# Performance work log

Measured on AMD Instinct MI355X. Metric: run time of the kernel, lower is better.

## Reference

```python
import jax, jax.numpy as jnp
import numpy as np

N_NODES = 50000
N_EDGES = 500000
D_MODEL = 128
D_INNER = 256
N_EXPERT = 64
TOP_K = 2
CAP_FACTOR = 2  # capacity factor for expert dispatch (fastmoe has no drop; factor 2 is ample for ~uniform gates)
BN_EPS = 1e-5


def setup_inputs() -> dict:
    key = jax.random.key(0)
    ks = jax.random.split(key, 12)
    d, h, E = D_MODEL, D_INNER, N_EXPERT
    return {
        "feats": jax.random.normal(ks[0], (N_NODES, d), jnp.float32),
        "edge_src": jax.random.randint(ks[1], (N_EDGES,), 0, N_NODES),
        "edge_dst": jax.random.randint(ks[2], (N_EDGES,), 0, N_NODES),
        "W_conv": jax.random.normal(ks[3], (d, d), jnp.float32) / np.sqrt(d),
        "b_conv": jnp.zeros((d,), jnp.float32),
        "gate_W": jax.random.normal(ks[4], (d, E), jnp.float32) / np.sqrt(d),
        "gate_b": jnp.zeros((E,), jnp.float32),
        "W1": jax.random.normal(ks[5], (E, d, h), jnp.float32) / np.sqrt(d),
        "b1": jnp.zeros((E, h), jnp.float32),
        "W2": jax.random.normal(ks[6], (E, h, d), jnp.float32) / np.sqrt(h),
        "b2": jnp.zeros((E, d), jnp.float32),
        "bn_gamma": jnp.ones((d,), jnp.float32),
        "bn_beta": jnp.zeros((d,), jnp.float32),
    }


def _gcn_conv(feats, edge_src, edge_dst, W_conv, b_conv):
    # symmetric-normalized sum aggregation over edge list
    n = feats.shape[0]
    ones = jnp.ones_like(edge_dst, dtype=feats.dtype)
    deg = jax.ops.segment_sum(ones, edge_dst, num_segments=n)
    deg = jnp.maximum(deg, 1.0)
    inv_sqrt = jax.lax.rsqrt(deg)
    norm = inv_sqrt[edge_src] * inv_sqrt[edge_dst]          # [Ed]
    msgs = feats[edge_src] * norm[:, None]                  # [Ed, d]
    agg = jax.ops.segment_sum(msgs, edge_dst, num_segments=n)
    return agg @ W_conv + b_conv


def _moe_ffn(x, gate_W, gate_b, W1, b1, W2, b2):
    # fastmoe NaiveGate: top-k of linear gate, softmax over the top-k scores
    T, d = x.shape
    E, h = W1.shape[0], W1.shape[2]
    scores = x @ gate_W + gate_b                            # [T, E]
    topv, topi = jax.lax.top_k(scores, TOP_K)               # [T, k]
    gw = jax.nn.softmax(topv, axis=-1)                      # [T, k]

    P = T * TOP_K
    eid = topi.reshape(P)                                   # expert id per (token, slot)
    x_rep = jnp.repeat(x, TOP_K, axis=0)                    # [P, d]

    onehot = jax.nn.one_hot(eid, E, dtype=jnp.int32)        # [P, E]
    pos = jnp.sum(jnp.cumsum(onehot, axis=0) * onehot, axis=-1) - 1  # rank within expert
    C = CAP_FACTOR * int(np.ceil(P / E))
    valid = pos < C
    slot = eid * C + jnp.where(valid, pos, 0)               # [P]

    buf = jnp.zeros((E * C, d), x.dtype).at[slot].add(
        jnp.where(valid[:, None], x_rep, 0.0))
    buf = buf.reshape(E, C, d)
    hact = jax.nn.gelu(jnp.einsum('ecd,edh->ech', buf, W1) + b1[:, None, :],
                       approximate=False)
    y = jnp.einsum('ech,ehd->ecd', hact, W2) + b2[:, None, :]
    y_pairs = y.reshape(E * C, d)[slot] * valid[:, None].astype(x.dtype)  # [P, d]
    y_pairs = y_pairs.reshape(T, TOP_K, d)
    return jnp.einsum('tk,tkd->td', gw, y_pairs)


def _batchnorm(x, gamma, beta):
    mean = jnp.mean(x, axis=0)
    var = jnp.mean(jnp.square(x - mean), axis=0)  # biased, as torch BN training
    return (x - mean) * jax.lax.rsqrt(var + BN_EPS) * gamma + beta


def reference(feats, edge_src, edge_dst, W_conv, b_conv, gate_W, gate_b,
              W1, b1, W2, b2, bn_gamma, bn_beta):
    new_feats = _gcn_conv(feats, edge_src, edge_dst, W_conv, b_conv)
    core = _moe_ffn(new_feats, gate_W, gate_b, W1, b1, W2, b2)
    # dropout p=0.0 -> identity; BN(inp + core_out)
    return _batchnorm(new_feats + core, bn_gamma, bn_beta)
```

## Files before the change

kernel.cpp:

```cpp
#include <hip/hip_runtime.h>
#include <math.h>

#define N_NODES 50000
#define N_EDGES 500000
#define D 128
#define H 256
#define NE 64
#define TOPK 2
#define NPAIR (N_NODES * TOPK)
#define CAP 3126
#define TILE_R 32
#define BQ 16
#define BN_NBLK 128
#define BN_ROWS ((N_NODES + BN_NBLK - 1) / BN_NBLK)

typedef __attribute__((ext_vector_type(8))) short s16x8;
typedef __attribute__((ext_vector_type(4))) float f32x4;

__device__ __forceinline__ unsigned short f2bf(float f) {
    unsigned u = __float_as_uint(f);
    unsigned r = (u + 0x7fffu + ((u >> 16) & 1u)) >> 16;
    return (unsigned short)r;
}
__device__ __forceinline__ float bf2f(unsigned short u) {
    return __uint_as_float(((unsigned)u) << 16);
}

__device__ __forceinline__ float gelu_f(float x) {
    float u = 0.70710678118654752f * x;
    float au = fabsf(u);
    float t = 1.0f / fmaf(0.3275911f, au, 1.0f);
    float poly = t * fmaf(t, fmaf(t, fmaf(t, fmaf(t, 1.061405429f, -1.453152027f),
                      1.421413741f), -0.284496736f), 0.254829592f);
    float e = __expf(-u * u);
    float erfa = 1.0f - poly * e;
    float erfu = copysignf(erfa, u);
    return 0.5f * x * (1.0f + erfu);
}

#define DOT2(s, c, xx, ww) {                      \
    float p_ = (xx) * (ww);                       \
    float e1_ = fmaf((xx), (ww), -p_);            \
    float t_ = (s) + p_;                          \
    float z_ = t_ - (s);                          \
    float e2_ = ((s) - (t_ - z_)) + (p_ - z_);    \
    (s) = t_;                                     \
    (c) += e1_ + e2_; }

#define TSUM(s, c, pp) {                          \
    float p_ = (pp);                              \
    float t_ = (s) + p_;                          \
    float z_ = t_ - (s);                          \
    float e2_ = ((s) - (t_ - z_)) + (p_ - z_);    \
    (s) = t_;                                     \
    (c) += e2_; }

#define KAH(s, c, pp) {                           \
    float y_ = (pp) - (c);                        \
    float t_ = (s) + y_;                          \
    (c) = (t_ - (s)) - y_;                        \
    (s) = t_; }

__global__ void k_deg(const int* __restrict__ dst, int* __restrict__ deg) {
    int i = blockIdx.x * blockDim.x + threadIdx.x;
    if (i < N_EDGES) atomicAdd(&deg[dst[i]], 1);
}

__global__ void k_invsqrt(const int* __restrict__ deg, float* __restrict__ invs) {
    int i = blockIdx.x * blockDim.x + threadIdx.x;
    if (i < N_NODES) {
        double d = (double)deg[i];
        if (d < 1.0) d = 1.0;
        invs[i] = (float)(1.0 / sqrt(d));
    }
}

__global__ __launch_bounds__(1024) void k_scan(const int* __restrict__ deg,
                                               int* __restrict__ rowptr) {
    __shared__ int sh[1024];
    int t = threadIdx.x;
    const int chunk = (N_NODES + 1023) / 1024;
    int lo = t * chunk;
    int hi = min(lo + chunk, N_NODES);
    int s = 0;
    for (int i = lo; i < hi; i++) s += deg[i];
    sh[t] = s;
    __syncthreads();
    for (int off = 1; off < 1024; off <<= 1) {
        int v = (t >= off) ? sh[t - off] : 0;
        __syncthreads();
        sh[t] += v;
        __syncthreads();
    }
    int run = (t == 0) ? 0 : sh[t - 1];
    for (int i = lo; i < hi; i++) { rowptr[i] = run; run += deg[i]; }
    if (t == 1023) rowptr[N_NODES] = run;
}

__global__ void k_scatter(const int* __restrict__ src, const int* __restrict__ dst,
                          const int* __restrict__ rowptr, int* __restrict__ cursor,
                          int* __restrict__ csr) {
    int e = blockIdx.x * blockDim.x + threadIdx.x;
    if (e >= N_EDGES) return;
    int d = dst[e];
    int pos = atomicAdd(&cursor[d], 1);
    csr[rowptr[d] + pos] = src[e];
}

__global__ __launch_bounds__(256) void k_gather(const float* __restrict__ feats,
                                                const int* __restrict__ rowptr,
                                                const int* __restrict__ csr,
                                                const float* __restrict__ invs,
                                                float* __restrict__ agg) {
    int node = blockIdx.x * 4 + (threadIdx.x >> 6);
    if (node >= N_NODES) return;
    int lane = threadIdx.x & 63;
    int beg = rowptr[node], end = rowptr[node + 1];
    float wd = invs[node];
    float sx = 0.f, cx = 0.f, sy = 0.f, cy = 0.f;
    int i = beg;
    for (; i + 4 <= end; i += 4) {
        int s0 = csr[i], s1 = csr[i + 1], s2 = csr[i + 2], s3 = csr[i + 3];
        float n0 = invs[s0] * wd, n1 = invs[s1] * wd;
        float n2 = invs[s2] * wd, n3 = invs[s3] * wd;
        float2 f0 = ((const float2*)(feats + (size_t)s0 * D))[lane];
        float2 f1 = ((const float2*)(feats + (size_t)s1 * D))[lane];
        float2 f2 = ((const float2*)(feats + (size_t)s2 * D))[lane];
        float2 f3 = ((const float2*)(feats + (size_t)s3 * D))[lane];
        KAH(sx, cx, n0 * f0.x); KAH(sy, cy, n0 * f0.y);
        KAH(sx, cx, n1 * f1.x); KAH(sy, cy, n1 * f1.y);
        KAH(sx, cx, n2 * f2.x); KAH(sy, cy, n2 * f2.y);
        KAH(sx, cx, n3 * f3.x); KAH(sy, cy, n3 * f3.y);
    }
    for (; i < end; i++) {
        int s = csr[i];
        float nrm = invs[s] * wd;
        float2 f = ((const float2*)(feats + (size_t)s * D))[lane];
        KAH(sx, cx, nrm * f.x);
        KAH(sy, cy, nrm * f.y);
    }
    ((float2*)(agg + (size_t)node * D))[lane] = make_float2(sx, sy);
}

__global__ __launch_bounds__(256) void k_wcsplit(const float* __restrict__ W,
                                                 unsigned short* __restrict__ whi,
                                                 unsigned short* __restrict__ wlo) {
    int u = blockIdx.x * 256 + threadIdx.x;
    int lhi = u & 3, c = (u >> 2) & 127, ks = u >> 9;
    int k0 = ks * 32 + lhi * 8;
    unsigned short vh[8] __attribute__((aligned(16)));
    unsigned short vl[8] __attribute__((aligned(16)));
#pragma unroll
    for (int j = 0; j < 8; j++) {
        float x = W[(size_t)(k0 + j) * D + c];
        unsigned short h = f2bf(x);
        vh[j] = h;
        vl[j] = f2bf(x - bf2f(h));
    }
    *(int4*)(whi + (size_t)u * 8) = *(int4*)vh;
    *(int4*)(wlo + (size_t)u * 8) = *(int4*)vl;
}

__global__ __launch_bounds__(512, 4) void k_conv(const float* __restrict__ agg,
                                                 const unsigned short* __restrict__ whi,
                                                 const unsigned short* __restrict__ wlo,
                                                 const float* __restrict__ bias,
                                                 float* __restrict__ out) {
    __shared__ __align__(16) char smem[32768];
    const int XH = 0, XL = 8192, YB = 16384;
    int r0 = blockIdx.x * TILE_R;
    int rows = min(TILE_R, N_NODES - r0);
    int tid = threadIdx.x;
    int wv = tid >> 6, lane = tid & 63;
    int lhi = lane >> 4, llo = lane & 15;
    int sr = tid >> 4, ss = tid & 15;
    f32x4 zero = {0.f, 0.f, 0.f, 0.f};

    int c = wv * 16 + llo;
    s16x8 whf[4], wlf[4];
#pragma unroll
    for (int ks = 0; ks < 4; ks++) {
        size_t u = ((size_t)(ks * 128 + c) * 4 + lhi) * 8;
        whf[ks] = *(const s16x8*)(whi + u);
        wlf[ks] = *(const s16x8*)(wlo + u);
    }

    {
        float v[8];
        if (sr < rows) {
            const float4* xr = (const float4*)(agg + (size_t)(r0 + sr) * D + ss * 8);
            *(float4*)(v + 0) = xr[0];
            *(float4*)(v + 4) = xr[1];
        } else {
#pragma unroll
            for (int k = 0; k < 8; k++) v[k] = 0.f;
        }
        unsigned short hb[8] __attribute__((aligned(16)));
        unsigned short lb[8] __attribute__((aligned(16)));
#pragma unroll
        for (int k = 0; k < 8; k++) {
            unsigned short h = f2bf(v[k]);
            hb[k] = h;
            lb[k] = f2bf(v[k] - bf2f(h));
        }
        int swz = (sr & 7) << 4;
        *(int4*)(smem + XH + sr * 256 + ((ss * 16) ^ swz)) = *(int4*)hb;
        *(int4*)(smem + XL + sr * 256 + ((ss * 16) ^ swz)) = *(int4*)lb;
    }
    __syncthreads();

    f32x4 acc[2];
    acc[0] = zero; acc[1] = zero;
#pragma unroll
    for (int ks = 0; ks < 4; ks++) {
        int kb = ks * 64 + lhi * 16;
        int sw0 = (llo & 7) << 4;
        s16x8 ah0 = *(const s16x8*)(smem + XH + llo * 256        + (kb ^ sw0));
        s16x8 ah1 = *(const s16x8*)(smem + XH + (llo + 16) * 256 + (kb ^ sw0));
        s16x8 al0 = *(const s16x8*)(smem + XL + llo * 256        + (kb ^ sw0));
        s16x8 al1 = *(const s16x8*)(smem + XL + (llo + 16) * 256 + (kb ^ sw0));
        acc[0] = __builtin_amdgcn_mfma_f32_16x16x32_bf16(ah0, whf[ks], acc[0], 0, 0, 0);
        acc[0] = __builtin_amdgcn_mfma_f32_16x16x32_bf16(ah0, wlf[ks], acc[0], 0, 0, 0);
        acc[0] = __builtin_amdgcn_mfma_f32_16x16x32_bf16(al0, whf[ks], acc[0], 0, 0, 0);
        acc[1] = __builtin_amdgcn_mfma_f32_16x16x32_bf16(ah1, whf[ks], acc[1], 0, 0, 0);
        acc[1] = __builtin_amdgcn_mfma_f32_16x16x32_bf16(ah1, wlf[ks], acc[1], 0, 0, 0);
        acc[1] = __builtin_amdgcn_mfma_f32_16x16x32_bf16(al1, whf[ks], acc[1], 0, 0, 0);
    }

    {
        float bb = bias[c];
#pragma unroll
        for (int mt = 0; mt < 2; mt++)
#pragma unroll
            for (int r = 0; r < 4; r++) {
                int m = mt * 16 + lhi * 4 + r;
                *(float*)(smem + YB + m * 512 + ((c * 4) ^ ((m & 7) << 4))) = acc[mt][r] + bb;
            }
    }
    __syncthreads();

    if (sr < rows) {
        int swz = (sr & 7) << 4;
        int4 a = *(const int4*)(smem + YB + sr * 512 + ((ss * 32) ^ swz));
        int4 b = *(const int4*)(smem + YB + sr * 512 + ((ss * 32 + 16) ^ swz));
        float4* op = (float4*)(out + (size_t)(r0 + sr) * D + ss * 8);
        op[0] = *(float4*)&a;
        op[1] = *(float4*)&b;
    }
}

__global__ __launch_bounds__(256, 4) void k_gate(const float* __restrict__ nf,
                                                 const float* __restrict__ gW,
                                                 const float* __restrict__ gb,
                                                 float* __restrict__ gwout,
                                                 int* __restrict__ topi,
                                                 int* __restrict__ rcnt,
                                                 int* __restrict__ redo) {
    __shared__ float Wl[D * NE];
    __shared__ float xsh[16 * D];
    for (int i = threadIdx.x; i < D * NE / 4; i += 256)
        ((float4*)Wl)[i] = ((const float4*)gW)[i];
    int t_base = blockIdx.x * 16;
    for (int i = threadIdx.x; i < 16 * 32; i += 256) {
        int r = i >> 5, q = i & 31;
        ((float4*)(xsh + r * D))[q] =
            ((const float4*)(nf + (size_t)(t_base + r) * D))[q];
    }
    __syncthreads();

    int wave = threadIdx.x >> 6;
    int lane = threadIdx.x & 63;
    int t0 = t_base + wave * 4;
    const float* xw = xsh + wave * 4 * D;

    float a0 = 0.f, a1 = 0.f, a2 = 0.f, a3 = 0.f;
#pragma unroll 4
    for (int k4 = 0; k4 < D; k4 += 4) {
        float x0[4], x1[4], x2[4], x3[4];
        *(float4*)x0 = *(const float4*)(xw + k4);
        *(float4*)x1 = *(const float4*)(xw + D + k4);
        *(float4*)x2 = *(const float4*)(xw + 2 * D + k4);
        *(float4*)x3 = *(const float4*)(xw + 3 * D + k4);
#pragma unroll
        for (int u = 0; u < 4; u++) {
            float w = Wl[(k4 + u) * NE + lane];
            a0 = fmaf(x0[u], w, a0);
            a1 = fmaf(x1[u], w, a1);
            a2 = fmaf(x2[u], w, a2);
            a3 = fmaf(x3[u], w, a3);
        }
    }
    float gbf = gb[lane];
    float af[4] = {a0 + gbf, a1 + gbf, a2 + gbf, a3 + gbf};

    const float TAU = 2e-4f;

#pragma unroll
    for (int j = 0; j < 4; j++) {
        float sf = (j == 0) ? af[0] : (j == 1) ? af[1] : (j == 2) ? af[2] : af[3];
        int t = t0 + j;

        float v1 = sf; int i1 = lane;
#pragma unroll
        for (int off = 32; off; off >>= 1) {
            float ov = __shfl_xor(v1, off);
            int   oi = __shfl_xor(i1, off);
            if (ov > v1 || (ov == v1 && oi < i1)) { v1 = ov; i1 = oi; }
        }
        float v2 = (lane == i1) ? -INFINITY : sf; int i2 = lane;
#pragma unroll
        for (int off = 32; off; off >>= 1) {
            float ov = __shfl_xor(v2, off);
            int   oi = __shfl_xor(i2, off);
            if (ov > v2 || (ov == v2 && oi < i2)) { v2 = ov; i2 = oi; }
        }
        float v3 = (lane == i1 || lane == i2) ? -INFINITY : sf;
#pragma unroll
        for (int off = 32; off; off >>= 1)
            v3 = fmaxf(v3, __shfl_xor(v3, off));

        if (lane == 0) {
            float dd = v2 - v1;
            float e2 = expf(dd);
            float g0 = 1.0f / (1.0f + e2);
            gwout[2 * t] = g0;
            gwout[2 * t + 1] = e2 * g0;
            topi[2 * t] = i1;
            topi[2 * t + 1] = i2;
            if ((v1 - v2 <= TAU) || (v2 - v3 <= TAU)) {
                int slot = atomicAdd(rcnt, 1);
                redo[slot] = t;
            }
        }
    }
}

__global__ __launch_bounds__(256) void k_gfix(const float* __restrict__ nf,
                                              const float* __restrict__ gW,
                                              const float* __restrict__ gb,
                                              const int* __restrict__ rcnt,
                                              const int* __restrict__ redo,
                                              float* __restrict__ gwout,
                                              int* __restrict__ topi) {
    int nredo = *rcnt;
    int lane = threadIdx.x & 63;
    int widx = blockIdx.x * 4 + (threadIdx.x >> 6);
    float gbf = gb[lane];
    for (int i = widx; i < nredo; i += gridDim.x * 4) {
        int t = redo[i];
        const float* xr = nf + (size_t)t * D;
        float s = 0.f, c = 0.f;
        for (int k = 0; k < D; k++)
            DOT2(s, c, xr[k], gW[k * NE + lane]);
        TSUM(s, c, gbf);
        float vv = s + c, rr = (s - vv) + c;

        float a1v = vv, a1r = rr; int i1 = lane;
#pragma unroll
        for (int off = 32; off; off >>= 1) {
            float ov = __shfl_xor(a1v, off);
            float orr = __shfl_xor(a1r, off);
            int   oi = __shfl_xor(i1, off);
            bool gt = (ov > a1v) || (ov == a1v && (orr > a1r || (orr == a1r && oi < i1)));
            if (gt) { a1v = ov; a1r = orr; i1 = oi; }
        }
        bool ex = (lane == i1);
        float a2v = ex ? -INFINITY : vv;
        float a2r = ex ? 0.f : rr;
        int i2 = lane;
#pragma unroll
        for (int off = 32; off; off >>= 1) {
            float ov = __shfl_xor(a2v, off);
            float orr = __shfl_xor(a2r, off);
            int   oi = __shfl_xor(i2, off);
            bool gt = (ov > a2v) || (ov == a2v && (orr > a2r || (orr == a2r && oi < i2)));
            if (gt) { a2v = ov; a2r = orr; i2 = oi; }
        }

        if (lane == 0) {
            float dd = (a2v - a1v) + (a2r - a1r);
            float e2 = expf(dd);
            float g0 = 1.0f / (1.0f + e2);
            gwout[2 * t] = g0;
            gwout[2 * t + 1] = e2 * g0;
            topi[2 * t] = i1;
            topi[2 * t + 1] = i2;
        }
    }
}

__global__ __launch_bounds__(1024) void k_disp(const int* __restrict__ topi,
                                               int* __restrict__ cnt,
                                               int* __restrict__ plist) {
    __shared__ int lcnt[NE];
    __shared__ int lbase[NE];
    int tid = threadIdx.x;
    if (tid < NE) lcnt[tid] = 0;
    __syncthreads();
    int p = blockIdx.x * 1024 + tid;
    int e = 0, lr = 0;
    bool act = (p < NPAIR);
    if (act) {
        e = topi[p];
        lr = atomicAdd(&lcnt[e], 1);
    }
    __syncthreads();
    if (tid < NE) {
        int n = lcnt[tid];
        lbase[tid] = n ? atomicAdd(&cnt[tid], n) : 0;
    }
    __syncthreads();
    if (act) {
        int slot = lbase[e] + lr;
        if (slot < CAP) plist[e * CAP + slot] = p;
    }
}

__global__ __launch_bounds__(256) void k_wconv(const float* __restrict__ W1,
                                               const float* __restrict__ W2,
                                               unsigned short* __restrict__ w1c,
                                               unsigned short* __restrict__ w2c) {
    int gid = blockIdx.x * 256 + threadIdx.x;
    const int NW1 = NE * 4 * 256 * 4;
    if (gid < NW1) {
        int lhi = gid & 3, h = (gid >> 2) & 255, ks = (gid >> 10) & 3, e = gid >> 12;
        int d0 = ks * 32 + lhi * 8;
        unsigned short v[8] __attribute__((aligned(16)));
#pragma unroll
        for (int j = 0; j < 8; j++)
            v[j] = f2bf(W1[((size_t)e * D + d0 + j) * H + h]);
        *(int4*)(w1c + (size_t)gid * 8) = *(int4*)v;
    } else {
        int g = gid - NW1;
        int lhi = g & 3, d = (g >> 2) & 127, ks = (g >> 9) & 7, e = g >> 12;
        int h0 = ks * 32 + lhi * 8;
        unsigned short v[8] __attribute__((aligned(16)));
#pragma unroll
        for (int j = 0; j < 8; j++)
            v[j] = f2bf(W2[((size_t)e * H + h0 + j) * D + d]);
        *(int4*)(w2c + (size_t)g * 8) = *(int4*)v;
    }
}

__global__ __launch_bounds__(512, 4) void k_moe(const float* __restrict__ nf,
                                                const int* __restrict__ cnt,
                                                const int* __restrict__ plist,
                                                const unsigned short* __restrict__ w1c,
                                                const float* __restrict__ b1,
                                                const unsigned short* __restrict__ w2c,
                                                const float* __restrict__ b2,
                                                const float* __restrict__ gwbuf,
                                                unsigned short* __restrict__ ybuf) {
    __shared__ __align__(16) char smem[32768];
    const int XA = 0, HL = 8192, YB = 24576;
    int e = blockIdx.x & 63;
    int q = blockIdx.x >> 6;
    int n = min(cnt[e], CAP);
    int ntile = (n + TILE_R - 1) / TILE_R;
    if (q >= ntile) return;
    int tid = threadIdx.x;

    int wv = tid >> 6, lane = tid & 63;
    int lhi = lane >> 4, llo = lane & 15;
    int sr = tid >> 4, ss = tid & 15;
    f32x4 zero = {0.f, 0.f, 0.f, 0.f};

    s16x8 w1f[4][2];
#pragma unroll
    for (int ks = 0; ks < 4; ks++)
#pragma unroll
        for (int nt = 0; nt < 2; nt++) {
            int h = wv * 32 + nt * 16 + llo;
            w1f[ks][nt] = *(const s16x8*)(w1c +
                ((size_t)e * 4096 + (ks * 256 + h) * 4 + lhi) * 8);
        }
    s16x8 w2f[8];
    {
        int d = wv * 16 + llo;
#pragma unroll
        for (int ks = 0; ks < 8; ks++)
            w2f[ks] = *(const s16x8*)(w2c +
                ((size_t)e * 4096 + (ks * 128 + d) * 4 + lhi) * 8);
    }

    float vals[8];
    auto loadt = [&](int rt2, float* v) {
        bool ok = false;
        if (rt2 < ntile) {
            int rows2 = min(TILE_R, n - rt2 * TILE_R);
            if (sr < rows2) {
                int p = plist[e * CAP + rt2 * TILE_R + sr];
                const float4* xr = (const float4*)(nf + (size_t)(p >> 1) * D + ss * 8);
                *(float4*)(v + 0) = xr[0];
                *(float4*)(v + 4) = xr[1];
                ok = true;
            }
        }
        if (!ok) {
#pragma unroll
            for (int k = 0; k < 8; k++) v[k] = 0.f;
        }
    };
    loadt(q, vals);

    for (int rt = q; rt < ntile; rt += BQ) {
        int r0 = rt * TILE_R;
        int rows = min(TILE_R, n - r0);

        {
            unsigned short hb[8] __attribute__((aligned(16)));
#pragma unroll
            for (int k = 0; k < 8; k++) hb[k] = f2bf(vals[k]);
            *(int4*)(smem + XA + sr * 256 + ((ss * 16) ^ ((sr & 7) << 4))) = *(int4*)hb;
        }
        __syncthreads();

        loadt(rt + BQ, vals);

        f32x4 acc1[2][2];
#pragma unroll
        for (int mt = 0; mt < 2; mt++)
#pragma unroll
            for (int nt = 0; nt < 2; nt++) acc1[mt][nt] = zero;
#pragma unroll
        for (int ks = 0; ks < 4; ks++) {
            int kb = ks * 64 + lhi * 16;
            s16x8 a0 = *(const s16x8*)(smem + XA + llo * 256        + (kb ^ ((llo & 7) << 4)));
            s16x8 a1 = *(const s16x8*)(smem + XA + (llo + 16) * 256 + (kb ^ ((llo & 7) << 4)));
#pragma unroll
            for (int nt = 0; nt < 2; nt++) {
                acc1[0][nt] = __builtin_amdgcn_mfma_f32_16x16x32_bf16(a0, w1f[ks][nt], acc1[0][nt], 0, 0, 0);
                acc1[1][nt] = __builtin_amdgcn_mfma_f32_16x16x32_bf16(a1, w1f[ks][nt], acc1[1][nt], 0, 0, 0);
            }
        }

#pragma unroll
        for (int mt = 0; mt < 2; mt++)
#pragma unroll
            for (int nt = 0; nt < 2; nt++)
#pragma unroll
                for (int r = 0; r < 4; r++) {
                    int m = mt * 16 + lhi * 4 + r;
                    int hc = wv * 32 + nt * 16 + llo;
                    float hv = acc1[mt][nt][r] + b1[e * H + hc];
                    *(unsigned short*)(smem + HL + m * 512 + ((hc * 2) ^ ((m & 7) << 4))) =
                        f2bf(gelu_f(hv));
                }
        __syncthreads();

        f32x4 acc2[2];
        acc2[0] = zero; acc2[1] = zero;
#pragma unroll
        for (int ks = 0; ks < 8; ks++) {
            int kb = ks * 64 + lhi * 16;
            s16x8 a0 = *(const s16x8*)(smem + HL + llo * 512        + (kb ^ ((llo & 7) << 4)));
            s16x8 a1 = *(const s16x8*)(smem + HL + (llo + 16) * 512 + (kb ^ ((llo & 7) << 4)));
            acc2[0] = __builtin_amdgcn_mfma_f32_16x16x32_bf16(a0, w2f[ks], acc2[0], 0, 0, 0);
            acc2[1] = __builtin_amdgcn_mfma_f32_16x16x32_bf16(a1, w2f[ks], acc2[1], 0, 0, 0);
        }

        {
            int d = wv * 16 + llo;
            float bb = b2[e * D + d];
#pragma unroll
            for (int mt = 0; mt < 2; mt++)
#pragma unroll
                for (int r = 0; r < 4; r++) {
                    int m = mt * 16 + lhi * 4 + r;
                    *(unsigned short*)(smem + YB + m * 256 + ((d * 2) ^ ((m & 7) << 4))) =
                        f2bf(acc2[mt][r] + bb);
                }
        }
        __syncthreads();

        if (sr < rows) {
            int p = plist[e * CAP + r0 + sr];
            float gw = gwbuf[p];
            unsigned short yv[8] __attribute__((aligned(16)));
            *(int4*)yv = *(const int4*)(smem + YB + sr * 256 + ((ss * 16) ^ ((sr & 7) << 4)));
#pragma unroll
            for (int k = 0; k < 8; k++) yv[k] = f2bf(gw * bf2f(yv[k]));
            *(int4*)(ybuf + (size_t)p * D + ss * 8) = *(int4*)yv;
        }
    }
}

__global__ __launch_bounds__(256) void k_bnpart(float* __restrict__ nf,
                                                const unsigned short* __restrict__ ybuf,
                                                double* __restrict__ part) {
    int blk = blockIdx.x;
    int col = threadIdx.x & 127;
    int half = threadIdx.x >> 7;
    int r0 = blk * BN_ROWS;
    int r1 = min(r0 + BN_ROWS, N_NODES);
    double s = 0.0, ss = 0.0;
    for (int r = r0 + half; r < r1; r += 2) {
        float v32 = nf[(size_t)r * D + col]
                  + bf2f(ybuf[(size_t)(2 * r) * D + col])
                  + bf2f(ybuf[(size_t)(2 * r + 1) * D + col]);
        nf[(size_t)r * D + col] = v32;
        double v = (double)v32;
        s += v; ss += v * v;
    }
    __shared__ double sh[2][256];
    sh[0][threadIdx.x] = s; sh[1][threadIdx.x] = ss;
    __syncthreads();
    if (threadIdx.x < 128) {
        part[(size_t)blk * 256 + col]       = sh[0][col] + sh[0][col + 128];
        part[(size_t)blk * 256 + 128 + col] = sh[1][col] + sh[1][col + 128];
    }
}

__global__ void k_bnstats(const double* __restrict__ part,
                          const float* __restrict__ gamma,
                          float* __restrict__ stats) {
    int col = threadIdx.x;
    double s = 0.0, ss = 0.0;
    for (int b = 0; b < BN_NBLK; b++) {
        s  += part[(size_t)b * 256 + col];
        ss += part[(size_t)b * 256 + 128 + col];
    }
    double mean = s / (double)N_NODES;
    double var = ss / (double)N_NODES - mean * mean;
    stats[col] = (float)mean;
    stats[128 + col] = gamma[col] * (float)(1.0 / sqrt(var + 1e-5));
}

__global__ __launch_bounds__(256) void k_bnapply(const float* __restrict__ stats,
                                                 const float* __restrict__ beta,
                                                 float* __restrict__ out) {
    int i = blockIdx.x * blockDim.x + threadIdx.x;
    if (i >= N_NODES * (D / 4)) return;
    int q = i & 31;
    int c0 = q * 4;
    float4 z = ((const float4*)out)[i];
    float4 r;
    r.x = (z.x - stats[c0 + 0]) * stats[128 + c0 + 0] + beta[c0 + 0];
    r.y = (z.y - stats[c0 + 1]) * stats[128 + c0 + 1] + beta[c0 + 1];
    r.z = (z.z - stats[c0 + 2]) * stats[128 + c0 + 2] + beta[c0 + 2];
    r.w = (z.w - stats[c0 + 3]) * stats[128 + c0 + 3] + beta[c0 + 3];
    ((float4*)out)[i] = r;
}

extern "C" void kernel_launch(void* const* d_in, const int* in_sizes, int n_in,
                              void* d_out, int out_size, void* d_ws, size_t ws_size,
                              hipStream_t stream) {
    const float* feats   = (const float*)d_in[0];
    const int*   esrc    = (const int*)d_in[1];
    const int*   edst    = (const int*)d_in[2];
    const float* W_conv  = (const float*)d_in[3];
    const float* b_conv  = (const float*)d_in[4];
    const float* gate_W  = (const float*)d_in[5];
    const float* gate_b  = (const float*)d_in[6];
    const float* W1      = (const float*)d_in[7];
    const float* b1      = (const float*)d_in[8];
    const float* W2      = (const float*)d_in[9];
    const float* b2      = (const float*)d_in[10];
    const float* bn_g    = (const float*)d_in[11];
    const float* bn_b    = (const float*)d_in[12];
    float* out = (float*)d_out;

    char* ws = (char*)d_ws;
    size_t off = 0;
    auto rup = [](size_t x) { return (x + 255) & ~(size_t)255; };
    int*    deg    = (int*)   (ws + off); off += rup((size_t)N_NODES * 4);
    int*    cursor = (int*)   (ws + off); off += rup((size_t)N_NODES * 4);
    int*    cnt    = (int*)   (ws + off); off += 256;
    int*    rcnt   = (int*)   (ws + off); off += 256;
    size_t zero_bytes = off;
    float*  invs   = (float*) (ws + off); off += rup((size_t)N_NODES * 4);
    int*    rowptr = (int*)   (ws + off); off += rup((size_t)(N_NODES + 1) * 4);
    int*    csr    = (int*)   (ws + off); off += rup((size_t)N_EDGES * 4);
    float*  gwbuf  = (float*) (ws + off); off += rup((size_t)NPAIR * 4);
    int*    topi   = (int*)   (ws + off); off += rup((size_t)NPAIR * 4);
    int*    redo   = (int*)   (ws + off); off += rup((size_t)N_NODES * 4);
    int*    plist  = (int*)   (ws + off); off += rup((size_t)NE * CAP * 4);
    double* part   = (double*)(ws + off); off += rup((size_t)BN_NBLK * 256 * 8);
    float*  stats  = (float*) (ws + off); off += 1024;
    unsigned short* w1c  = (unsigned short*)(ws + off); off += rup((size_t)NE * D * H * 2);
    unsigned short* w2c  = (unsigned short*)(ws + off); off += rup((size_t)NE * D * H * 2);
    unsigned short* wchi = (unsigned short*)(ws + off); off += rup((size_t)D * D * 2);
    unsigned short* wclo = (unsigned short*)(ws + off); off += rup((size_t)D * D * 2);
    unsigned short* ybuf = (unsigned short*)(ws + off); off += rup((size_t)NPAIR * D * 2);
    float*  agg    = (float*)ybuf;
    (void)ws_size; (void)in_sizes; (void)n_in; (void)out_size;

    hipMemsetAsync(d_ws, 0, zero_bytes, stream);

    k_wconv<<<2 * NE * 4 * 256 * 4 / 256, 256, 0, stream>>>(W1, W2, w1c, w2c);
    k_wcsplit<<<8, 256, 0, stream>>>(W_conv, wchi, wclo);
    k_deg<<<(N_EDGES + 255) / 256, 256, 0, stream>>>(edst, deg);
    k_invsqrt<<<(N_NODES + 255) / 256, 256, 0, stream>>>(deg, invs);
    k_scan<<<1, 1024, 0, stream>>>(deg, rowptr);
    k_scatter<<<(N_EDGES + 255) / 256, 256, 0, stream>>>(esrc, edst, rowptr, cursor, csr);
    k_gather<<<(N_NODES + 3) / 4, 256, 0, stream>>>(feats, rowptr, csr, invs, agg);
    k_conv<<<(N_NODES + TILE_R - 1) / TILE_R, 512, 0, stream>>>(agg, wchi, wclo, b_conv, out);
    k_gate<<<N_NODES / 16, 256, 0, stream>>>(out, gate_W, gate_b, gwbuf, topi, rcnt, redo);
    k_gfix<<<128, 256, 0, stream>>>(out, gate_W, gate_b, rcnt, redo, gwbuf, topi);
    k_disp<<<(NPAIR + 1023) / 1024, 1024, 0, stream>>>(topi, cnt, plist);
    k_moe<<<NE * BQ, 512, 0, stream>>>(out, cnt, plist, w1c, b1, w2c, b2, gwbuf, ybuf);
    k_bnpart<<<BN_NBLK, 256, 0, stream>>>(out, ybuf, part);
    k_bnstats<<<1, 128, 0, stream>>>(part, bn_g, stats);
    k_bnapply<<<(N_NODES * (D / 4) + 255) / 256, 256, 0, stream>>>(stats, bn_b, out);
}
```

Before: 417.7 us.

## Fuse gate scoring into conv kernel using split-bf16 MFMA

```diff
diff --git a/kernel.cpp b/kernel.cpp
--- a/kernel.cpp
+++ b/kernel.cpp
@@ -161,13 +161,35 @@
     *(int4*)(wlo + (size_t)u * 8) = *(int4*)vl;
 }
 
-__global__ __launch_bounds__(512, 4) void k_conv(const float* __restrict__ agg,
-                                                 const unsigned short* __restrict__ whi,
-                                                 const unsigned short* __restrict__ wlo,
-                                                 const float* __restrict__ bias,
-                                                 float* __restrict__ out) {
+__global__ __launch_bounds__(256) void k_wgsplit(const float* __restrict__ gW,
+                                                 unsigned short* __restrict__ ghi,
+                                                 unsigned short* __restrict__ glo) {
+    int u = blockIdx.x * 256 + threadIdx.x;
+    int lhi = u & 3, e = (u >> 2) & 63, ks = u >> 8;
+    int k0 = ks * 32 + lhi * 8;
+    unsigned short vh[8] __attribute__((aligned(16)));
+    unsigned short vl[8] __attribute__((aligned(16)));
+#pragma unroll
+    for (int j = 0; j < 8; j++) {
+        float x = gW[(size_t)(k0 + j) * NE + e];
+        unsigned short h = f2bf(x);
+        vh[j] = h;
+        vl[j] = f2bf(x - bf2f(h));
+    }
+    *(int4*)(ghi + (size_t)u * 8) = *(int4*)vh;
+    *(int4*)(glo + (size_t)u * 8) = *(int4*)vl;
+}
+
+__global__ __launch_bounds__(512, 4) void k_convgate(
+        const float* __restrict__ agg,
+        const unsigned short* __restrict__ whi, const unsigned short* __restrict__ wlo,
+        const float* __restrict__ bias,
+        const unsigned short* __restrict__ ghi, const unsigned short* __restrict__ glo,
+        const float* __restrict__ gb,
+        float* __restrict__ out, float* __restrict__ gwout, int* __restrict__ topi,
+        int* __restrict__ rcnt, int* __restrict__ redo) {
     __shared__ __align__(16) char smem[32768];
-    const int XH = 0, XL = 8192, YB = 16384;
+    const int XH = 0, XL = 8192, YB = 16384, SC = 16384;
     int r0 = blockIdx.x * TILE_R;
     int rows = min(TILE_R, N_NODES - r0);
     int tid = threadIdx.x;
@@ -183,6 +205,15 @@
         size_t u = ((size_t)(ks * 128 + c) * 4 + lhi) * 8;
         whf[ks] = *(const s16x8*)(whi + u);
         wlf[ks] = *(const s16x8*)(wlo + u);
+    }
+    s16x8 gwh[4], gwl[4];
+    if (wv < 4) {
+#pragma unroll
+        for (int ks = 0; ks < 4; ks++) {
+            size_t u = ((size_t)(ks * 64 + c) * 4 + lhi) * 8;
+            gwh[ks] = *(const s16x8*)(ghi + u);
+            gwl[ks] = *(const s16x8*)(glo + u);
+        }
     }
 
     {
@@ -226,6 +257,7 @@
         acc[1] = __builtin_amdgcn_mfma_f32_16x16x32_bf16(ah1, wlf[ks], acc[1], 0, 0, 0);
         acc[1] = __builtin_amdgcn_mfma_f32_16x16x32_bf16(al1, whf[ks], acc[1], 0, 0, 0);
     }
+    __syncthreads();
 
     {
         float bb = bias[c];
@@ -234,7 +266,12 @@
 #pragma unroll
             for (int r = 0; r < 4; r++) {
                 int m = mt * 16 + lhi * 4 + r;
-                *(float*)(smem + YB + m * 512 + ((c * 4) ^ ((m & 7) << 4))) = acc[mt][r] + bb;
+                float ov = acc[mt][r] + bb;
+                int swz = (m & 7) << 4;
+                *(float*)(smem + YB + m * 512 + ((c * 4) ^ swz)) = ov;
+                unsigned short h = f2bf(ov);
+                *(unsigned short*)(smem + XH + m * 256 + ((c * 2) ^ swz)) = h;
+                *(unsigned short*)(smem + XL + m * 256 + ((c * 2) ^ swz)) = f2bf(ov - bf2f(h));
             }
     }
     __syncthreads();
@@ -247,58 +284,46 @@
         op[0] = *(float4*)&a;
         op[1] = *(float4*)&b;
     }
-}
-
-__global__ __launch_bounds__(256, 4) void k_gate(const float* __restrict__ nf,
-                                                 const float* __restrict__ gW,
-                                                 const float* __restrict__ gb,
-                                                 float* __restrict__ gwout,
-                                                 int* __restrict__ topi,
-                                                 int* __restrict__ rcnt,
-                                                 int* __restrict__ redo) {
-    __shared__ float Wl[D * NE];
-    __shared__ float xsh[16 * D];
-    for (int i = threadIdx.x; i < D * NE / 4; i += 256)
-        ((float4*)Wl)[i] = ((const float4*)gW)[i];
-    int t_base = blockIdx.x * 16;
-    for (int i = threadIdx.x; i < 16 * 32; i += 256) {
-        int r = i >> 5, q = i & 31;
-        ((float4*)(xsh + r * D))[q] =
-            ((const float4*)(nf + (size_t)(t_base + r) * D))[q];
-    }
-    __syncthreads();
-
-    int wave = threadIdx.x >> 6;
-    int lane = threadIdx.x & 63;
-    int t0 = t_base + wave * 4;
-    const float* xw = xsh + wave * 4 * D;
-
-    float a0 = 0.f, a1 = 0.f, a2 = 0.f, a3 = 0.f;
-#pragma unroll 4
-    for (int k4 = 0; k4 < D; k4 += 4) {
-        float x0[4], x1[4], x2[4], x3[4];
-        *(float4*)x0 = *(const float4*)(xw + k4);
-        *(float4*)x1 = *(const float4*)(xw + D + k4);
-        *(float4*)x2 = *(const float4*)(xw + 2 * D + k4);
-        *(float4*)x3 = *(const float4*)(xw + 3 * D + k4);
-#pragma unroll
-        for (int u = 0; u < 4; u++) {
-            float w = Wl[(k4 + u) * NE + lane];
-            a0 = fmaf(x0[u], w, a0);
-            a1 = fmaf(x1[u], w, a1);
-            a2 = fmaf(x2[u], w, a2);
-            a3 = fmaf(x3[u], w, a3);
-        }
-    }
-    float gbf = gb[lane];
-    float af[4] = {a0 + gbf, a1 + gbf, a2 + gbf, a3 + gbf};
+    f32x4 accg[2];
+    accg[0] = zero; accg[1] = zero;
+    if (wv < 4) {
+#pragma unroll
+        for (int ks = 0; ks < 4; ks++) {
+            int kb = ks * 64 + lhi * 16;
+            int sw0 = (llo & 7) << 4;
+            s16x8 ah0 = *(const s16x8*)(smem + XH + llo * 256        + (kb ^ sw0));
+            s16x8 ah1 = *(const s16x8*)(smem + XH + (llo + 16) * 256 + (kb ^ sw0));
+            s16x8 al0 = *(const s16x8*)(smem + XL + llo * 256        + (kb ^ sw0));
+            s16x8 al1 = *(const s16x8*)(smem + XL + (llo + 16) * 256 + (kb ^ sw0));
+            accg[0] = __builtin_amdgcn_mfma_f32_16x16x32_bf16(ah0, gwh[ks], accg[0], 0, 0, 0);
+            accg[0] = __builtin_amdgcn_mfma_f32_16x16x32_bf16(ah0, gwl[ks], accg[0], 0, 0, 0);
+            accg[0] = __builtin_amdgcn_mfma_f32_16x16x32_bf16(al0, gwh[ks], accg[0], 0, 0, 0);
+            accg[1] = __builtin_amdgcn_mfma_f32_16x16x32_bf16(ah1, gwh[ks], accg[1], 0, 0, 0);
+            accg[1] = __builtin_amdgcn_mfma_f32_16x16x32_bf16(ah1, gwl[ks], accg[1], 0, 0, 0);
+            accg[1] = __builtin_amdgcn_mfma_f32_16x16x32_bf16(al1, gwh[ks], accg[1], 0, 0, 0);
+        }
+    }
+    __syncthreads();
+
+    if (wv < 4) {
+        float gbe = gb[c];
+#pragma unroll
+        for (int mt = 0; mt < 2; mt++)
+#pragma unroll
+            for (int r = 0; r < 4; r++) {
+                int m = mt * 16 + lhi * 4 + r;
+                *(float*)(smem + SC + m * 256 + c * 4) = accg[mt][r] + gbe;
+            }
+    }
+    __syncthreads();
 
     const float TAU = 2e-4f;
-
 #pragma unroll
     for (int j = 0; j < 4; j++) {
-        float sf = (j == 0) ? af[0] : (j == 1) ? af[1] : (j == 2) ? af[2] : af[3];
-        int t = t0 + j;
+        int tt = wv * 4 + j;
+        if (tt >= rows) break;
+        int t = r0 + tt;
+        float sf = *(const float*)(smem + SC + tt * 256 + lane * 4);
 
         float v1 = sf; int i1 = lane;
 #pragma unroll
@@ -681,6 +706,8 @@
     unsigned short* w2c  = (unsigned short*)(ws + off); off += rup((size_t)NE * D * H * 2);
     unsigned short* wchi = (unsigned short*)(ws + off); off += rup((size_t)D * D * 2);
     unsigned short* wclo = (unsigned short*)(ws + off); off += rup((size_t)D * D * 2);
+    unsigned short* wghi = (unsigned short*)(ws + off); off += rup((size_t)D * NE * 2);
+    unsigned short* wglo = (unsigned short*)(ws + off); off += rup((size_t)D * NE * 2);
     unsigned short* ybuf = (unsigned short*)(ws + off); off += rup((size_t)NPAIR * D * 2);
     float*  agg    = (float*)ybuf;
     (void)ws_size; (void)in_sizes; (void)n_in; (void)out_size;
@@ -689,13 +716,14 @@
 
     k_wconv<<<2 * NE * 4 * 256 * 4 / 256, 256, 0, stream>>>(W1, W2, w1c, w2c);
     k_wcsplit<<<8, 256, 0, stream>>>(W_conv, wchi, wclo);
+    k_wgsplit<<<4, 256, 0, stream>>>(gate_W, wghi, wglo);
     k_deg<<<(N_EDGES + 255) / 256, 256, 0, stream>>>(edst, deg);
     k_invsqrt<<<(N_NODES + 255) / 256, 256, 0, stream>>>(deg, invs);
     k_scan<<<1, 1024, 0, stream>>>(deg, rowptr);
     k_scatter<<<(N_EDGES + 255) / 256, 256, 0, stream>>>(esrc, edst, rowptr, cursor, csr);
     k_gather<<<(N_NODES + 3) / 4, 256, 0, stream>>>(feats, rowptr, csr, invs, agg);
-    k_conv<<<(N_NODES + TILE_R - 1) / TILE_R, 512, 0, stream>>>(agg, wchi, wclo, b_conv, out);
-    k_gate<<<N_NODES / 16, 256, 0, stream>>>(out, gate_W, gate_b, gwbuf, topi, rcnt, redo);
+    k_convgate<<<(N_NODES + TILE_R - 1) / TILE_R, 512, 0, stream>>>(
+        agg, wchi, wclo, b_conv, wghi, wglo, gate_b, out, gwbuf, topi, rcnt, redo);
     k_gfix<<<128, 256, 0, stream>>>(out, gate_W, gate_b, rcnt, redo, gwbuf, topi);
     k_disp<<<(NPAIR + 1023) / 1024, 1024, 0, stream>>>(topi, cnt, plist);
     k_moe<<<NE * BQ, 512, 0, stream>>>(out, cnt, plist, w1c, b1, w2c, b2, gwbuf, ybuf);
```

Result: faster. 402.0 us (median of 2 runs) (-3.8%).
